# Kernel tuning notes

Measured on AMD Instinct MI355X. Metric: run time of the kernel, lower is better.

The kernel has to match this reference:

```python
import jax, jax.numpy as jnp
import numpy as np

SPARSE_COMPRESSION_RATIO = 0.5  # config.sparse_compression_ratio


def setup_inputs() -> dict:
    key = jax.random.key(0)
    kv_cache = jax.random.normal(key, (2, 32, 4096, 128), dtype=jnp.float32)
    return {"kv_cache": kv_cache}


def reference(kv_cache):
    # elements_to_keep = int(numel * (1 - ratio))
    total = kv_cache.size
    k = int(total * (1.0 - SPARSE_COMPRESSION_RATIO))
    flat = kv_cache.reshape(-1)
    # torch.topk(|x|, k, largest=True) -> indices of k largest magnitudes
    _, top_idx = jax.lax.top_k(jnp.abs(flat), k)
    # scatter mask, then elementwise multiply (zeros out non-top-k entries)
    mask = jnp.zeros((total,), dtype=jnp.bool_).at[top_idx].set(True)
    return kv_cache * mask.reshape(kv_cache.shape)
```

## Files before the change

kernel.cpp:

```cpp
#include <hip/hip_runtime.h>
#include <stdint.h>


#define NTHR 256
#define MASK31 0x7fffffffu

typedef unsigned int v4u __attribute__((ext_vector_type(4)));

#define SH_OFF    0
#define SH_BINS   8192
#define CH_OFF    8192
#define CH_BINS   4096
#define SCL_OFF   12288
#define ZERO_WORDS (SCL_OFF + 32)
#define HIC_OFF   12320
#define PCN_OFF   14368
#define L3C_OFF   16416
#define L3S_OFF   16672
#define L3SEG_CAP 64
#define OVFP_OFF  49440
#define OVFP_CAP  16384
#define OVL3_OFF  90000
#define OVL3_CAP  2048
#define PAIRS_OFF 131072
#define SEG_CAP   2048
#define NBLK_MAIN 2048

__global__ void zero_ws_kernel(uint32_t* __restrict__ ws) {
    int i = blockIdx.x * blockDim.x + threadIdx.x;
    if (i < ZERO_WORDS) ws[i] = 0;
}

__global__ void sample_hist_kernel(const v4u* __restrict__ xv, long long n4,
                                   uint32_t* __restrict__ ws) {
    __shared__ uint32_t lh[SH_BINS];
    for (int i = threadIdx.x; i < SH_BINS; i += NTHR) lh[i] = 0;
    __syncthreads();
    long long S4 = n4 >> 3;
    long long T = (long long)gridDim.x * NTHR;
    for (long long s = (long long)blockIdx.x * NTHR + threadIdx.x; s < S4; s += T) {
        long long idx4 = ((s >> 9) << 12) | (s & 511);
        if (idx4 < n4) {
            v4u v = xv[idx4];
            atomicAdd(&lh[(v.x & MASK31) >> 18], 1u);
            atomicAdd(&lh[(v.y & MASK31) >> 18], 1u);
            atomicAdd(&lh[(v.z & MASK31) >> 18], 1u);
            atomicAdd(&lh[(v.w & MASK31) >> 18], 1u);
        }
    }
    __syncthreads();
    for (int i = threadIdx.x; i < SH_BINS; i += NTHR)
        if (lh[i]) atomicAdd(&ws[SH_OFF + i], lh[i]);
}

__global__ void sel_bracket_kernel(uint32_t* __restrict__ ws,
                                   uint32_t ksmM, uint32_t kspM) {
    __shared__ uint32_t lh[SH_BINS];
    __shared__ uint32_t csum[NTHR];
    __shared__ uint32_t cpre[NTHR];
    __shared__ int sBHi, sB1;
    for (int i = threadIdx.x; i < SH_BINS; i += NTHR) lh[i] = ws[SH_OFF + i];
    if (threadIdx.x == 0) { sBHi = -1; sB1 = -1; }
    __syncthreads();
    uint32_t s = 0;
    for (int i = 0; i < 32; ++i) s += lh[threadIdx.x * 32 + i];
    csum[threadIdx.x] = s;
    __syncthreads();
    if (threadIdx.x == 0) {
        uint32_t run = 0;
        for (int c = NTHR - 1; c >= 0; --c) { cpre[c] = run; run += csum[c]; }
    }
    __syncthreads();
    {
        int c = threadIdx.x;
        int hitHi = -1, hitB1 = -1;
        uint32_t excl = cpre[c];
        for (int bb = c * 32 + 31; bb >= c * 32; --bb) {
            uint32_t cnt = lh[bb];
            uint32_t incl = excl + cnt;
            if (hitHi < 0 && incl >= ksmM) hitHi = bb;
            if (hitB1 < 0 && excl >= kspM) hitB1 = bb;
            excl = incl;
        }
        if (hitHi >= 0) atomicMax(&sBHi, hitHi);
        if (hitB1 >= 0) atomicMax(&sB1, hitB1);
    }
    __syncthreads();
    if (threadIdx.x == 0) {
        int bHi = sBHi < 0 ? 0 : sBHi;
        int bLo = sB1 + 1;
        if (bLo > bHi) bLo = bHi;
        if (bLo < 0) bLo = 0;
        int sbins = bHi - bLo + 1;
        int clog = 0; while ((1 << clog) < sbins) ++clog;
        int spanBits = 18 + clog;
        int shift1 = spanBits - 12;
        if (shift1 < 0) shift1 = 0;
        ws[SCL_OFF + 0] = ((uint32_t)bLo) << 18;
        ws[SCL_OFF + 1] = ((uint32_t)(bHi + 1)) << 18;
        ws[SCL_OFF + 2] = (uint32_t)shift1;
    }
}

__global__ void fused_main_kernel(const uint32_t* __restrict__ x,
                                  uint32_t* __restrict__ out, long long n,
                                  uint32_t* __restrict__ ws) {
    __shared__ uint2 stage[SEG_CAP];
    __shared__ uint32_t cnt, redHi[NTHR / 64];
    const uint32_t uLo = ws[SCL_OFF + 0];
    const uint32_t uHi = ws[SCL_OFF + 1];
    const uint32_t span = uHi - uLo;
    if (threadIdx.x == 0) cnt = 0u;
    __syncthreads();

    const v4u* __restrict__ xv = (const v4u*)x;
    v4u* __restrict__ ov = (v4u*)out;
    long long n4 = n >> 2;
    const long long stride = (long long)gridDim.x * NTHR;
    const long long i0 = (long long)blockIdx.x * NTHR + threadIdx.x;

    uint32_t myHi = 0;
    uint32_t hitMask = 0;
    uint32_t it = 0;

    for (long long i = i0; i < n4; i += stride, ++it) {
        v4u v = xv[i];
        uint32_t c0 = v.x & MASK31, c1 = v.y & MASK31;
        uint32_t c2 = v.z & MASK31, c3 = v.w & MASK31;
        myHi += (uint32_t)(c0 >= uHi) + (uint32_t)(c1 >= uHi)
              + (uint32_t)(c2 >= uHi) + (uint32_t)(c3 >= uHi);
        v4u o;
        o.x = (c0 >= uHi) ? v.x : 0u;
        o.y = (c1 >= uHi) ? v.y : 0u;
        o.z = (c2 >= uHi) ? v.z : 0u;
        o.w = (c3 >= uHi) ? v.w : 0u;
        uint32_t hb = (uint32_t)((c0 - uLo) < span) | (uint32_t)((c1 - uLo) < span)
                    | (uint32_t)((c2 - uLo) < span) | (uint32_t)((c3 - uLo) < span);
        hitMask |= hb << (it & 31);
        ov[i] = o;
    }

    uint2* __restrict__ ovfp = (uint2*)(ws + OVFP_OFF);
#define PUSHP(val, eidx) { \
    uint32_t p_ = atomicAdd(&cnt, 1u); \
    uint2 pr_ = make_uint2((val), (eidx)); \
    if (p_ < SEG_CAP) stage[p_] = pr_; \
    else { uint32_t g_ = atomicAdd(&ws[SCL_OFF + 5], 1u); \
           if (g_ < OVFP_CAP) ovfp[g_] = pr_; } }

    if (blockIdx.x == 0) {
        for (long long idx = (n4 << 2) + threadIdx.x; idx < n; idx += NTHR) {
            uint32_t v = x[idx];
            uint32_t u = v & MASK31;
            myHi += (uint32_t)(u >= uHi);
            if (u - uLo < span) PUSHP(v, (uint32_t)idx)
            out[idx] = (u >= uHi) ? v : 0u;
        }
    }

    while (hitMask) {
        uint32_t b = __ffs(hitMask) - 1u;
        hitMask &= hitMask - 1u;
        for (long long ii = i0 + (long long)b * stride; ii < n4; ii += (stride << 5)) {
            v4u v = xv[ii];
            uint32_t e0 = (uint32_t)(ii << 2);
            uint32_t u;
            u = v.x & MASK31; if (u - uLo < span) PUSHP(v.x, e0 + 0u)
            u = v.y & MASK31; if (u - uLo < span) PUSHP(v.y, e0 + 1u)
            u = v.z & MASK31; if (u - uLo < span) PUSHP(v.z, e0 + 2u)
            u = v.w & MASK31; if (u - uLo < span) PUSHP(v.w, e0 + 3u)
        }
    }
#undef PUSHP

    for (int o = 32; o > 0; o >>= 1) myHi += __shfl_down(myHi, o);
    if ((threadIdx.x & 63) == 0) redHi[threadIdx.x >> 6] = myHi;
    __syncthreads();
    if (threadIdx.x == 0) {
        uint32_t tot = 0;
        for (int w = 0; w < NTHR / 64; ++w) tot += redHi[w];
        ws[HIC_OFF + blockIdx.x] = tot;
        uint32_t c = cnt < SEG_CAP ? cnt : SEG_CAP;
        cnt = c;
        ws[PCN_OFF + blockIdx.x] = c;
    }
    __syncthreads();
    uint2* __restrict__ seg = (uint2*)(ws + PAIRS_OFF) + (size_t)blockIdx.x * SEG_CAP;
    uint32_t c = cnt;
    for (uint32_t q = threadIdx.x; q < c; q += NTHR) seg[q] = stage[q];
}

__global__ void cand_hist_kernel(uint32_t* __restrict__ ws) {
    __shared__ uint32_t lh[CH_BINS];
    uint32_t uLo = ws[SCL_OFF + 0], shift1 = ws[SCL_OFF + 2];
    for (int i = threadIdx.x; i < CH_BINS; i += NTHR) lh[i] = 0;
    __syncthreads();
    const uint2* pairs = (const uint2*)(ws + PAIRS_OFF);
    for (int g = 0; g < NBLK_MAIN / 256; ++g) {
        uint32_t sidx = blockIdx.x + (uint32_t)g * 256u;
        uint32_t c = ws[PCN_OFF + sidx];
        const uint2* seg = pairs + (size_t)sidx * SEG_CAP;
        for (uint32_t i = threadIdx.x; i < c; i += NTHR) {
            uint32_t u = seg[i].x & MASK31;
            atomicAdd(&lh[((u - uLo) >> shift1) & (CH_BINS - 1)], 1u);
        }
    }
    if (blockIdx.x == 0) {
        uint32_t c = ws[SCL_OFF + 5]; if (c > OVFP_CAP) c = OVFP_CAP;
        const uint2* ovfp = (const uint2*)(ws + OVFP_OFF);
        for (uint32_t i = threadIdx.x; i < c; i += NTHR) {
            uint32_t u = ovfp[i].x & MASK31;
            atomicAdd(&lh[((u - uLo) >> shift1) & (CH_BINS - 1)], 1u);
        }
    }
    __syncthreads();
    for (int i = threadIdx.x; i < CH_BINS; i += NTHR)
        if (lh[i]) atomicAdd(&ws[CH_OFF + i], lh[i]);
}

__global__ void sel_gather_kernel(uint32_t* __restrict__ ws, uint32_t k) {
    __shared__ uint32_t lh[CH_BINS];
    __shared__ uint32_t csum[NTHR];
    __shared__ uint32_t cpre[NTHR];
    __shared__ uint32_t sBase2, sRem2, sKp, lcnt;
    uint32_t part = 0;
    for (int i = threadIdx.x; i < NBLK_MAIN; i += NTHR) part += ws[HIC_OFF + i];
    for (int o = 32; o > 0; o >>= 1) part += __shfl_down(part, o);
    for (int i = threadIdx.x; i < CH_BINS; i += NTHR) lh[i] = ws[CH_OFF + i];
    if (threadIdx.x == 0) lcnt = 0;
    csum[threadIdx.x] = 0;
    __syncthreads();
    if ((threadIdx.x & 63) == 0) csum[threadIdx.x >> 6] = part;
    __syncthreads();
    uint32_t cntHi = csum[0] + csum[1] + csum[2] + csum[3];
    __syncthreads();
    uint32_t s = 0;
    for (int i = 0; i < 16; ++i) s += lh[threadIdx.x * 16 + i];
    csum[threadIdx.x] = s;
    __syncthreads();
    if (threadIdx.x == 0) {
        uint32_t run = 0;
        for (int c = NTHR - 1; c >= 0; --c) { cpre[c] = run; run += csum[c]; }
        uint32_t total = cpre[0] + csum[0];
        uint32_t kp = (k > cntHi) ? (k - cntHi) : 1u;
        if (kp > total) kp = total;
        if (kp < 1u) kp = 1u;
        sKp = kp;
    }
    __syncthreads();
    uint32_t kp = sKp;
    if (cpre[threadIdx.x] < kp && kp <= cpre[threadIdx.x] + csum[threadIdx.x]) {
        uint32_t excl = cpre[threadIdx.x];
        for (int bb = threadIdx.x * 16 + 15; bb >= threadIdx.x * 16; --bb) {
            uint32_t cnt = lh[bb];
            if (excl + cnt >= kp) {
                sBase2 = ws[SCL_OFF + 0] + (((uint32_t)bb) << ws[SCL_OFF + 2]);
                sRem2 = kp - excl;
                break;
            }
            excl += cnt;
        }
    }
    __syncthreads();
    if (threadIdx.x == 0) { ws[SCL_OFF + 3] = sBase2; ws[SCL_OFF + 4] = sRem2; }
    uint32_t base2 = sBase2;
    uint32_t width = 1u << ws[SCL_OFF + 2];
    const uint2* pairs = (const uint2*)(ws + PAIRS_OFF);
    uint2* myl3 = (uint2*)(ws + L3S_OFF) + (size_t)blockIdx.x * L3SEG_CAP;
    uint2* ovl3 = (uint2*)(ws + OVL3_OFF);
    __shared__ uint2 lstage[L3SEG_CAP];
    for (int g = 0; g < NBLK_MAIN / 256; ++g) {
        uint32_t sidx = blockIdx.x + (uint32_t)g * 256u;
        uint32_t c = ws[PCN_OFF + sidx];
        const uint2* seg = pairs + (size_t)sidx * SEG_CAP;
        for (uint32_t i = threadIdx.x; i < c; i += NTHR) {
            uint2 pr = seg[i];
            if ((pr.x & MASK31) - base2 < width) {
                uint32_t p = atomicAdd(&lcnt, 1u);
                if (p < L3SEG_CAP) lstage[p] = pr;
                else { uint32_t g2 = atomicAdd(&ws[SCL_OFF + 6], 1u);
                       if (g2 < OVL3_CAP) ovl3[g2] = pr; }
            }
        }
    }
    if (blockIdx.x == 0) {
        uint32_t c = ws[SCL_OFF + 5]; if (c > OVFP_CAP) c = OVFP_CAP;
        const uint2* ovfp = (const uint2*)(ws + OVFP_OFF);
        for (uint32_t i = threadIdx.x; i < c; i += NTHR) {
            uint2 pr = ovfp[i];
            if ((pr.x & MASK31) - base2 < width) {
                uint32_t p = atomicAdd(&lcnt, 1u);
                if (p < L3SEG_CAP) lstage[p] = pr;
                else { uint32_t g2 = atomicAdd(&ws[SCL_OFF + 6], 1u);
                       if (g2 < OVL3_CAP) ovl3[g2] = pr; }
            }
        }
    }
    __syncthreads();
    uint32_t c = lcnt < L3SEG_CAP ? lcnt : L3SEG_CAP;
    if (threadIdx.x == 0) ws[L3C_OFF + blockIdx.x] = c;
    for (uint32_t q = threadIdx.x; q < c; q += NTHR) myl3[q] = lstage[q];
}

#define L3TOT_CAP 4096
__global__ void final_fixup_kernel(uint32_t* __restrict__ ws,
                                   uint32_t* __restrict__ out) {
    __shared__ uint2 l3s[L3TOT_CAP];
    __shared__ uint32_t tc;
    uint32_t base2 = ws[SCL_OFF + 3], rem2 = ws[SCL_OFF + 4];
    uint32_t width = 1u << ws[SCL_OFF + 2];
    uint32_t tHi2 = base2 + width;
    if (threadIdx.x == 0) tc = 0;
    __syncthreads();
    const uint2* l3seg = (const uint2*)(ws + L3S_OFF);
    for (int s2 = threadIdx.x; s2 < 256; s2 += NTHR) {
        uint32_t c = ws[L3C_OFF + s2];
        uint32_t p = atomicAdd(&tc, c);
        for (uint32_t q = 0; q < c; ++q)
            if (p + q < L3TOT_CAP) l3s[p + q] = l3seg[(size_t)s2 * L3SEG_CAP + q];
    }
    if (threadIdx.x == 0) {
        uint32_t c = ws[SCL_OFF + 6]; if (c > OVL3_CAP) c = OVL3_CAP;
        uint32_t p = atomicAdd(&tc, c);
        const uint2* ovl3 = (const uint2*)(ws + OVL3_OFF);
        for (uint32_t q = 0; q < c; ++q)
            if (p + q < L3TOT_CAP) l3s[p + q] = ovl3[q];
    }
    __syncthreads();
    uint32_t c3 = tc < L3TOT_CAP ? tc : L3TOT_CAP;
    const uint2* pairs = (const uint2*)(ws + PAIRS_OFF);
    for (int g = 0; g < NBLK_MAIN / 256; ++g) {
        uint32_t sidx = blockIdx.x + (uint32_t)g * 256u;
        uint32_t c = ws[PCN_OFF + sidx];
        const uint2* seg = pairs + (size_t)sidx * SEG_CAP;
        for (uint32_t i = threadIdx.x; i < c; i += NTHR) {
            uint2 pr = seg[i];
            uint32_t u = pr.x & MASK31;
            if (u >= tHi2) {
                out[pr.y] = pr.x;
            } else if (u - base2 < width) {
                uint32_t rank = 0;
                for (uint32_t p = 0; p < c3; ++p) {
                    uint2 q2 = l3s[p];
                    uint32_t up = q2.x & MASK31;
                    rank += (up > u || (up == u && q2.y < pr.y)) ? 1u : 0u;
                }
                if (rank < rem2) out[pr.y] = pr.x;
            }
        }
    }
    if (blockIdx.x == 0) {
        uint32_t c = ws[SCL_OFF + 5]; if (c > OVFP_CAP) c = OVFP_CAP;
        const uint2* ovfp = (const uint2*)(ws + OVFP_OFF);
        for (uint32_t i = threadIdx.x; i < c; i += NTHR) {
            uint2 pr = ovfp[i];
            uint32_t u = pr.x & MASK31;
            if (u >= tHi2) {
                out[pr.y] = pr.x;
            } else if (u - base2 < width) {
                uint32_t rank = 0;
                for (uint32_t p = 0; p < c3; ++p) {
                    uint2 q2 = l3s[p];
                    uint32_t up = q2.x & MASK31;
                    rank += (up > u || (up == u && q2.y < pr.y)) ? 1u : 0u;
                }
                if (rank < rem2) out[pr.y] = pr.x;
            }
        }
    }
}

extern "C" void kernel_launch(void* const* d_in, const int* in_sizes, int n_in,
                              void* d_out, int out_size, void* d_ws, size_t ws_size,
                              hipStream_t stream) {
    const uint32_t* x = (const uint32_t*)d_in[0];
    uint32_t* out = (uint32_t*)d_out;
    uint32_t* ws = (uint32_t*)d_ws;
    long long n = (long long)in_sizes[0];

    const double ratio = 0.5;
    long long k = (long long)((double)n * (1.0 - ratio));
    if (k < 1) k = 1;
    if (k > n) k = n;

    long long n4 = n >> 2;
    long long S4 = n4 >> 3;
    long long S = S4 << 2;
    long long ks = (long long)((double)k * ((double)S / (double)n));
    const long long M = 9216;
    uint32_t ksmM = (uint32_t)((ks - M) < 1 ? 1 : (ks - M));
    uint32_t kspM = (uint32_t)((ks + M) > S ? S : (ks + M));

    zero_ws_kernel<<<(ZERO_WORDS + NTHR - 1) / NTHR, NTHR, 0, stream>>>(ws);
    sample_hist_kernel<<<256, NTHR, 0, stream>>>((const v4u*)x, n4, ws);
    sel_bracket_kernel<<<1, NTHR, 0, stream>>>(ws, ksmM, kspM);
    fused_main_kernel<<<NBLK_MAIN, NTHR, 0, stream>>>(x, out, n, ws);
    cand_hist_kernel<<<256, NTHR, 0, stream>>>(ws);
    sel_gather_kernel<<<256, NTHR, 0, stream>>>(ws, (uint32_t)k);
    final_fixup_kernel<<<256, NTHR, 0, stream>>>(ws, out);
}
```

Measured before the change: 145.0 us.

## Capture candidates in registers during streaming pass and sparsify histogram sample

The main streaming kernel now records up to four in-bracket candidates per thread in registers, so the second pass that re-reads global memory is only needed for threads with more hits. The sampling histogram reads a quarter as many elements, with a bracket margin scaled to the new sample size. The main grid is doubled with smaller per-block segments and the workspace offsets are re-laid out to match. Risks: a sparser sample gives a wider bracket and more candidates, and the extra capture logic adds register pressure and divergence to the hot loop.

```diff
diff --git a/kernel.cpp b/kernel.cpp
--- a/kernel.cpp
+++ b/kernel.cpp
@@ -1,5 +1,6 @@
 #include <hip/hip_runtime.h>
 #include <stdint.h>
+#include <math.h>
 
 
 #define NTHR 256
@@ -14,17 +15,18 @@
 #define SCL_OFF   12288
 #define ZERO_WORDS (SCL_OFF + 32)
 #define HIC_OFF   12320
-#define PCN_OFF   14368
-#define L3C_OFF   16416
-#define L3S_OFF   16672
+#define PCN_OFF   16416
+#define L3C_OFF   20512
+#define L3S_OFF   20768
 #define L3SEG_CAP 64
-#define OVFP_OFF  49440
+#define OVFP_OFF  53536
 #define OVFP_CAP  16384
-#define OVL3_OFF  90000
+#define OVL3_OFF  86304
 #define OVL3_CAP  2048
 #define PAIRS_OFF 131072
-#define SEG_CAP   2048
-#define NBLK_MAIN 2048
+#define SEG_CAP   1024
+#define NBLK_MAIN 4096
+#define STG_CAP   1024
 
 __global__ void zero_ws_kernel(uint32_t* __restrict__ ws) {
     int i = blockIdx.x * blockDim.x + threadIdx.x;
@@ -36,10 +38,10 @@
     __shared__ uint32_t lh[SH_BINS];
     for (int i = threadIdx.x; i < SH_BINS; i += NTHR) lh[i] = 0;
     __syncthreads();
-    long long S4 = n4 >> 3;
+    long long S4 = n4 >> 5;
     long long T = (long long)gridDim.x * NTHR;
     for (long long s = (long long)blockIdx.x * NTHR + threadIdx.x; s < S4; s += T) {
-        long long idx4 = ((s >> 9) << 12) | (s & 511);
+        long long idx4 = ((s >> 9) << 14) | (s & 511);
         if (idx4 < n4) {
             v4u v = xv[idx4];
             atomicAdd(&lh[(v.x & MASK31) >> 18], 1u);
@@ -105,7 +107,7 @@
 __global__ void fused_main_kernel(const uint32_t* __restrict__ x,
                                   uint32_t* __restrict__ out, long long n,
                                   uint32_t* __restrict__ ws) {
-    __shared__ uint2 stage[SEG_CAP];
+    __shared__ uint2 stage[STG_CAP];
     __shared__ uint32_t cnt, redHi[NTHR / 64];
     const uint32_t uLo = ws[SCL_OFF + 0];
     const uint32_t uHi = ws[SCL_OFF + 1];
@@ -121,6 +123,9 @@
 
     uint32_t myHi = 0;
     uint32_t hitMask = 0;
+    uint32_t myCnt = 0;
+    uint32_t s0v = 0, s0i = 0, s1v = 0, s1i = 0;
+    uint32_t s2v = 0, s2i = 0, s3v = 0, s3i = 0;
     uint32_t it = 0;
 
     for (long long i = i0; i < n4; i += stride, ++it) {
@@ -134,9 +139,25 @@
         o.y = (c1 >= uHi) ? v.y : 0u;
         o.z = (c2 >= uHi) ? v.z : 0u;
         o.w = (c3 >= uHi) ? v.w : 0u;
-        uint32_t hb = (uint32_t)((c0 - uLo) < span) | (uint32_t)((c1 - uLo) < span)
-                    | (uint32_t)((c2 - uLo) < span) | (uint32_t)((c3 - uLo) < span);
-        hitMask |= hb << (it & 31);
+        uint32_t h0 = (c0 - uLo) < span ? 1u : 0u;
+        uint32_t h1 = (c1 - uLo) < span ? 1u : 0u;
+        uint32_t h2 = (c2 - uLo) < span ? 1u : 0u;
+        uint32_t h3 = (c3 - uLo) < span ? 1u : 0u;
+        if (h0 | h1 | h2 | h3) {
+            hitMask |= 1u << (it & 31);
+            uint32_t e0 = (uint32_t)(i << 2);
+#define CAPT(hx, val, eidx) if (hx) { \
+    if (myCnt == 0)      { s0v = (val); s0i = (eidx); } \
+    else if (myCnt == 1) { s1v = (val); s1i = (eidx); } \
+    else if (myCnt == 2) { s2v = (val); s2i = (eidx); } \
+    else if (myCnt == 3) { s3v = (val); s3i = (eidx); } \
+    ++myCnt; }
+            CAPT(h0, v.x, e0 + 0u)
+            CAPT(h1, v.y, e0 + 1u)
+            CAPT(h2, v.z, e0 + 2u)
+            CAPT(h3, v.w, e0 + 3u)
+#undef CAPT
+        }
         ov[i] = o;
     }
 
@@ -144,7 +165,7 @@
 #define PUSHP(val, eidx) { \
     uint32_t p_ = atomicAdd(&cnt, 1u); \
     uint2 pr_ = make_uint2((val), (eidx)); \
-    if (p_ < SEG_CAP) stage[p_] = pr_; \
+    if (p_ < STG_CAP) stage[p_] = pr_; \
     else { uint32_t g_ = atomicAdd(&ws[SCL_OFF + 5], 1u); \
            if (g_ < OVFP_CAP) ovfp[g_] = pr_; } }
 
@@ -158,17 +179,24 @@
         }
     }
 
-    while (hitMask) {
-        uint32_t b = __ffs(hitMask) - 1u;
-        hitMask &= hitMask - 1u;
-        for (long long ii = i0 + (long long)b * stride; ii < n4; ii += (stride << 5)) {
-            v4u v = xv[ii];
-            uint32_t e0 = (uint32_t)(ii << 2);
-            uint32_t u;
-            u = v.x & MASK31; if (u - uLo < span) PUSHP(v.x, e0 + 0u)
-            u = v.y & MASK31; if (u - uLo < span) PUSHP(v.y, e0 + 1u)
-            u = v.z & MASK31; if (u - uLo < span) PUSHP(v.z, e0 + 2u)
-            u = v.w & MASK31; if (u - uLo < span) PUSHP(v.w, e0 + 3u)
+    if (myCnt <= 4u) {
+        if (myCnt > 0u) PUSHP(s0v, s0i)
+        if (myCnt > 1u) PUSHP(s1v, s1i)
+        if (myCnt > 2u) PUSHP(s2v, s2i)
+        if (myCnt > 3u) PUSHP(s3v, s3i)
+    } else {
+        while (hitMask) {
+            uint32_t b = __ffs(hitMask) - 1u;
+            hitMask &= hitMask - 1u;
+            for (long long ii = i0 + (long long)b * stride; ii < n4; ii += (stride << 5)) {
+                v4u v = xv[ii];
+                uint32_t e0 = (uint32_t)(ii << 2);
+                uint32_t u;
+                u = v.x & MASK31; if (u - uLo < span) PUSHP(v.x, e0 + 0u)
+                u = v.y & MASK31; if (u - uLo < span) PUSHP(v.y, e0 + 1u)
+                u = v.z & MASK31; if (u - uLo < span) PUSHP(v.z, e0 + 2u)
+                u = v.w & MASK31; if (u - uLo < span) PUSHP(v.w, e0 + 3u)
+            }
         }
     }
 #undef PUSHP
@@ -180,7 +208,7 @@
         uint32_t tot = 0;
         for (int w = 0; w < NTHR / 64; ++w) tot += redHi[w];
         ws[HIC_OFF + blockIdx.x] = tot;
-        uint32_t c = cnt < SEG_CAP ? cnt : SEG_CAP;
+        uint32_t c = cnt < STG_CAP ? cnt : STG_CAP;
         cnt = c;
         ws[PCN_OFF + blockIdx.x] = c;
     }
@@ -384,10 +412,10 @@
     if (k > n) k = n;
 
     long long n4 = n >> 2;
-    long long S4 = n4 >> 3;
-    long long S = S4 << 2;
+    long long S = (n4 >> 5) << 2;
+    if (S < 4) S = (n4 << 2);
     long long ks = (long long)((double)k * ((double)S / (double)n));
-    const long long M = 9216;
+    long long M = (long long)(9.0 * sqrt((double)S * 0.25)) + 64;
     uint32_t ksmM = (uint32_t)((ks - M) < 1 ? 1 : (ks - M));
     uint32_t kspM = (uint32_t)((ks + M) > S ? S : (ks + M));
 
```

After: 144.8 us. Within noise of the previous version (-0.1%).
